# Kernel optimization log

Measured on AMD Instinct MI355X. Metric: run time of the kernel, lower is better.

The kernel has to match this reference:

```python
import jax, jax.numpy as jnp
import numpy as np

BN_EPS = 1e-5


def conv1x1(x, w, b):
    # x: [B,C,H,W], w: [O,C] (squeezed 1x1 kernel), b: [O]
    return jnp.einsum('bchw,oc->bohw', x, w) + b[None, :, None, None]


def setup_inputs() -> dict:
    key = jax.random.key(0)
    ks = jax.random.split(key, 12)
    B, C, H, W = 4, 64, 256, 256
    s = 1.0 / np.sqrt(C).astype(np.float32)
    inp = {
        'x': jax.random.normal(ks[0], (B, C, H, W), jnp.float32),
        'theta_w': jax.random.normal(ks[1], (C, C), jnp.float32) * s,
        'theta_b': jax.random.normal(ks[2], (C,), jnp.float32) * 0.01,
        'phi_w': jax.random.normal(ks[3], (C, C), jnp.float32) * s,
        'phi_b': jax.random.normal(ks[4], (C,), jnp.float32) * 0.01,
        'g_w': jax.random.normal(ks[5], (C, C), jnp.float32) * s,
        'g_b': jax.random.normal(ks[6], (C,), jnp.float32) * 0.01,
        'w_w': jax.random.normal(ks[7], (C, C), jnp.float32) * s,
        'w_b': jax.random.normal(ks[8], (C,), jnp.float32) * 0.01,
        'bn_gamma': jax.random.normal(ks[9], (C,), jnp.float32) * 0.1,
        'bn_beta': jax.random.normal(ks[10], (C,), jnp.float32) * 0.1,
    }
    return inp


def reference(x, theta_w, theta_b, phi_w, phi_b, g_w, g_b, w_w, w_b, bn_gamma, bn_beta):
    B, C, H, W = x.shape
    N = H * W
    g_x = conv1x1(x, g_w, g_b).reshape(B, C, N)          # [B,C,N]
    theta_x = conv1x1(x, theta_w, theta_b).reshape(B, C, N)
    phi_x = conv1x1(x, phi_w, phi_b).reshape(B, C, N)
    # f = phi_x @ theta_x^T : channel-channel affinity [B,C,C]
    f = jnp.einsum('bcn,bdn->bcd', phi_x, theta_x)
    attn = jax.nn.softmax(f, axis=-1)                    # [B,C,C]
    y = jnp.einsum('bcd,bdn->bcn', attn, g_x)            # [B,C,N]
    # faithful to torch: permute(0,2,1).contiguous().view(B,C,H,W)
    y = jnp.transpose(y, (0, 2, 1)).reshape(B, C, H, W)
    w_y = conv1x1(y, w_w, w_b)                           # [B,C,H,W]
    # BatchNorm2d in training mode: batch stats over (B,H,W), biased var
    mean = jnp.mean(w_y, axis=(0, 2, 3), keepdims=True)
    var = jnp.var(w_y, axis=(0, 2, 3), keepdims=True)
    w_y = (w_y - mean) * jax.lax.rsqrt(var + BN_EPS)
    w_y = w_y * bn_gamma[None, :, None, None] + bn_beta[None, :, None, None]
    return w_y + x
```

## Files before the change

kernel.cpp:

```cpp
#include <hip/hip_runtime.h>
#include <hip/hip_bf16.h>
#include <stdint.h>

namespace {

constexpr size_t OFF_G     = 0;
constexpr size_t OFF_S     = 65536;
constexpr size_t OFF_M     = 66560;
constexpr size_t OFF_AB    = 132096;
constexpr size_t OFF_SCALE = 133120;
constexpr size_t OFF_STATS = 133632;
constexpr size_t OFF_WWT   = 134144;
constexpr size_t OFF_WSUM  = 150528;
constexpr size_t OFF_SPART = 150784;
constexpr size_t OFF_GPART = 412928;
constexpr size_t OFF_V     = 17190144;
constexpr size_t OFF_WY    = 50744576;

__device__ __forceinline__ float bf2f(unsigned short u) {
    return __uint_as_float(((unsigned)u) << 16);
}
__device__ __forceinline__ unsigned short f2bf(float f) {
    union { __hip_bfloat16 h; unsigned short u; } cv;
    cv.h = __float2bfloat16(f);
    return cv.u;
}
__device__ __forceinline__ unsigned pack2bf(float a, float b) {
    return (unsigned)f2bf(a) | ((unsigned)f2bf(b) << 16);
}

__global__ __launch_bounds__(256) void k_trans(const float* __restrict__ Ww,
                                               float* __restrict__ WwT,
                                               float* __restrict__ Wsum) {
    const int t = threadIdx.x;
    for (int e = t; e < 4096; e += 256) {
        const int o = e >> 6, c = e & 63;
        WwT[c * 64 + o] = Ww[e];
    }
    if (t < 64) {
        float s = 0.f;
#pragma unroll 8
        for (int c = 0; c < 64; ++c) s += Ww[t * 64 + c];
        Wsum[t] = s;
    }
}

__global__ __launch_bounds__(128) void k_gram(const float* __restrict__ x,
                                              float* __restrict__ gpart,
                                              float* __restrict__ spart) {
    const int wg = blockIdx.x;
    const int b = wg >> 8;
    const int chunk = wg & 255;
    const int t = threadIdx.x;
    const int wv = t >> 6;
    const int l = t & 63;
    const int g = l >> 3, h = l & 7;

    __shared__ __align__(16) float tile[64][64];
    __shared__ __align__(16) float Gred[4096];

    float acc[8][8];
#pragma unroll
    for (int i = 0; i < 8; ++i)
#pragma unroll
        for (int j = 0; j < 8; ++j) acc[i][j] = 0.f;
    float sp[8];
#pragma unroll
    for (int i = 0; i < 8; ++i) sp[i] = 0.f;

    const float* xb = x + (size_t)b * 64 * 65536 + chunk * 256;

    for (int t4 = 0; t4 < 4; ++t4) {
#pragma unroll
        for (int it = 0; it < 8; ++it) {
            const int v = it * 128 + t;
            const int row = v >> 4;
            const int c4 = v & 15;
            const float4 val = *(const float4*)(xb + (size_t)row * 65536 + t4 * 64 + c4 * 4);
            const int c4s = c4 ^ (row >> 3);
            *(float4*)&tile[row][c4s * 4] = val;
            sp[it] += val.x + val.y + val.z + val.w;
        }
        __syncthreads();
        const int fbase = wv * 8;
#pragma unroll
        for (int fs = 0; fs < 8; ++fs) {
            const int f = fbase + fs;
            float4 a4[8], b4[8];
#pragma unroll
            for (int i = 0; i < 8; ++i) a4[i] = *(const float4*)&tile[g * 8 + i][(f ^ g) * 4];
#pragma unroll
            for (int j = 0; j < 8; ++j) b4[j] = *(const float4*)&tile[h * 8 + j][(f ^ h) * 4];
#pragma unroll
            for (int i = 0; i < 8; ++i)
#pragma unroll
                for (int j = 0; j < 8; ++j) {
                    acc[i][j] += a4[i].x * b4[j].x;
                    acc[i][j] += a4[i].y * b4[j].y;
                    acc[i][j] += a4[i].z * b4[j].z;
                    acc[i][j] += a4[i].w * b4[j].w;
                }
        }
        __syncthreads();
    }

    if (wv == 1) {
#pragma unroll
        for (int i = 0; i < 8; ++i)
#pragma unroll
            for (int j4 = 0; j4 < 2; ++j4) {
                float4 v;
                v.x = acc[i][j4 * 4 + 0]; v.y = acc[i][j4 * 4 + 1];
                v.z = acc[i][j4 * 4 + 2]; v.w = acc[i][j4 * 4 + 3];
                *(float4*)&Gred[(g * 8 + i) * 64 + h * 8 + j4 * 4] = v;
            }
    }
    __syncthreads();
    if (wv == 0) {
        float* gp = gpart + (size_t)wg * 4096;
#pragma unroll
        for (int i = 0; i < 8; ++i)
#pragma unroll
            for (int j4 = 0; j4 < 2; ++j4) {
                const float4 r = *(const float4*)&Gred[(g * 8 + i) * 64 + h * 8 + j4 * 4];
                float4 v;
                v.x = acc[i][j4 * 4 + 0] + r.x; v.y = acc[i][j4 * 4 + 1] + r.y;
                v.z = acc[i][j4 * 4 + 2] + r.z; v.w = acc[i][j4 * 4 + 3] + r.w;
                *(float4*)(gp + (g * 8 + i) * 64 + h * 8 + j4 * 4) = v;
            }
    }
#pragma unroll
    for (int it = 0; it < 8; ++it) {
        float v = sp[it];
        v += __shfl_xor(v, 1);
        v += __shfl_xor(v, 2);
        v += __shfl_xor(v, 4);
        v += __shfl_xor(v, 8);
        if ((l & 15) == 0) {
            const int row = it * 8 + (t >> 4);
            spart[((size_t)b * 256 + chunk) * 64 + row] = v;
        }
    }
}

__global__ __launch_bounds__(256) void k_gred(const float* __restrict__ gpart,
                                              const float* __restrict__ spart,
                                              float* __restrict__ G,
                                              float* __restrict__ s) {
    const int b = blockIdx.x >> 4;
    const int part = blockIdx.x & 15;
    const int t = threadIdx.x;
    const int e4l = t & 63;
    const int cg = t >> 6;
    const int e4 = part * 64 + e4l;
    const float4* gp4 = (const float4*)gpart;

    float4 a = make_float4(0.f, 0.f, 0.f, 0.f);
#pragma unroll 8
    for (int i = 0; i < 64; ++i) {
        const int w = cg * 64 + i;
        const float4 v = gp4[((size_t)b * 256 + w) * 1024 + e4];
        a.x += v.x; a.y += v.y; a.z += v.z; a.w += v.w;
    }
    __shared__ __align__(16) float4 red[4][64];
    __shared__ float reds[4][64];
    red[cg][e4l] = a;

    float sv = 0.f;
    if (part == 0) {
#pragma unroll 8
        for (int i = 0; i < 64; ++i) {
            const int w = cg * 64 + i;
            sv += spart[((size_t)b * 256 + w) * 64 + e4l];
        }
        reds[cg][e4l] = sv;
    }
    __syncthreads();
    if (cg == 0) {
        const float4 r1 = red[1][e4l], r2 = red[2][e4l], r3 = red[3][e4l];
        float4 o;
        o.x = a.x + r1.x + r2.x + r3.x;
        o.y = a.y + r1.y + r2.y + r3.y;
        o.z = a.z + r1.z + r2.z + r3.z;
        o.w = a.w + r1.w + r2.w + r3.w;
        *(float4*)(G + (size_t)b * 4096 + (size_t)e4 * 4) = o;
        if (part == 0) {
            s[b * 64 + e4l] = sv + reds[1][e4l] + reds[2][e4l] + reds[3][e4l];
        }
    }
}

__global__ __launch_bounds__(256) void k_small(const float* __restrict__ G,
                                               const float* __restrict__ s,
                                               const float* __restrict__ Pw,
                                               const float* __restrict__ pb,
                                               const float* __restrict__ Tw,
                                               const float* __restrict__ tb,
                                               const float* __restrict__ Gw,
                                               const float* __restrict__ gb,
                                               float* __restrict__ Mt,
                                               float* __restrict__ ab) {
    const int b = blockIdx.x >> 1;
    const int rblk = (blockIdx.x & 1) * 32;
    const int t = threadIdx.x;
    const int rl = t >> 3;
    const int seg = t & 7;
    const int d0 = seg * 8;
    const int rg = rblk + rl;

    __shared__ __align__(16) float GL[64][68];
    __shared__ __align__(16) float TwL[64][68];
    __shared__ __align__(16) float GwL[64][68];
    __shared__ __align__(16) float PwL[32][68];
    __shared__ __align__(16) float AL[32][68];
    __shared__ __align__(16) float atL[32][68];
    __shared__ float sL[64], TsL[64], PsL[32], pbL[64], tbL[64], gbL[64];

    for (int v = t; v < 1024; v += 256) {
        const int k = v >> 4, c4 = (v & 15) * 4;
        *(float4*)&GL[k][c4]  = *(const float4*)(G + (size_t)b * 4096 + (size_t)v * 4);
        *(float4*)&TwL[k][c4] = *(const float4*)(Tw + (size_t)v * 4);
        *(float4*)&GwL[k][c4] = *(const float4*)(Gw + (size_t)v * 4);
    }
    for (int v = t; v < 512; v += 256) {
        const int k = v >> 4, c4 = (v & 15) * 4;
        *(float4*)&PwL[k][c4] = *(const float4*)(Pw + (size_t)(rblk + k) * 64 + c4);
    }
    if (t < 64) {
        sL[t] = s[b * 64 + t];
        pbL[t] = pb[t]; tbL[t] = tb[t]; gbL[t] = gb[t];
    }
    __syncthreads();
    if (t < 64) {
        float a = 0.f;
#pragma unroll 8
        for (int k = 0; k < 64; ++k) a += TwL[t][k] * sL[k];
        TsL[t] = a;
    }
    if (t < 32) {
        float a = 0.f;
#pragma unroll 8
        for (int k = 0; k < 64; ++k) a += PwL[t][k] * sL[k];
        PsL[t] = a;
    }
    {
        float4 a1 = make_float4(0.f, 0.f, 0.f, 0.f), a2 = make_float4(0.f, 0.f, 0.f, 0.f);
#pragma unroll 4
        for (int k = 0; k < 64; ++k) {
            const float pw = PwL[rl][k];
            const float4 g1 = *(const float4*)&GL[k][d0];
            const float4 g2 = *(const float4*)&GL[k][d0 + 4];
            a1.x += pw * g1.x; a1.y += pw * g1.y; a1.z += pw * g1.z; a1.w += pw * g1.w;
            a2.x += pw * g2.x; a2.y += pw * g2.y; a2.z += pw * g2.z; a2.w += pw * g2.w;
        }
        *(float4*)&AL[rl][d0] = a1;
        *(float4*)&AL[rl][d0 + 4] = a2;
    }
    __syncthreads();
    float4 areg[16];
#pragma unroll
    for (int i = 0; i < 16; ++i) areg[i] = *(const float4*)&AL[rl][i * 4];
    float fv[8];
#pragma unroll
    for (int dd = 0; dd < 8; ++dd) {
        const int d = d0 + dd;
        float4 a4 = make_float4(0.f, 0.f, 0.f, 0.f);
#pragma unroll
        for (int i = 0; i < 16; ++i) {
            const float4 tw = *(const float4*)&TwL[d][i * 4];
            a4.x += areg[i].x * tw.x; a4.y += areg[i].y * tw.y;
            a4.z += areg[i].z * tw.z; a4.w += areg[i].w * tw.w;
        }
        const float dot = (a4.x + a4.y) + (a4.z + a4.w);
        fv[dd] = dot + PsL[rl] * tbL[d] + pbL[rg] * (TsL[d] + 65536.f * tbL[d]);
    }
    float mx = fv[0];
#pragma unroll
    for (int dd = 1; dd < 8; ++dd) mx = fmaxf(mx, fv[dd]);
    mx = fmaxf(mx, __shfl_xor(mx, 1));
    mx = fmaxf(mx, __shfl_xor(mx, 2));
    mx = fmaxf(mx, __shfl_xor(mx, 4));
    float sm = 0.f;
#pragma unroll
    for (int dd = 0; dd < 8; ++dd) { fv[dd] = __expf(fv[dd] - mx); sm += fv[dd]; }
    sm += __shfl_xor(sm, 1);
    sm += __shfl_xor(sm, 2);
    sm += __shfl_xor(sm, 4);
    const float inv = 1.f / sm;
    float4 p1, p2;
    p1.x = fv[0] * inv; p1.y = fv[1] * inv; p1.z = fv[2] * inv; p1.w = fv[3] * inv;
    p2.x = fv[4] * inv; p2.y = fv[5] * inv; p2.z = fv[6] * inv; p2.w = fv[7] * inv;
    *(float4*)&atL[rl][d0] = p1;
    *(float4*)&atL[rl][d0 + 4] = p2;
    __syncthreads();
#pragma unroll
    for (int i = 0; i < 16; ++i) areg[i] = *(const float4*)&atL[rl][i * 4];
    float4 m1 = make_float4(0.f, 0.f, 0.f, 0.f), m2 = make_float4(0.f, 0.f, 0.f, 0.f);
    float abv = 0.f;
#pragma unroll
    for (int d4 = 0; d4 < 16; ++d4) {
        const float4 a = areg[d4];
#define MSTEP(comp, dc) { \
        const int d = d4 * 4 + dc; \
        const float ad = a.comp; \
        const float4 g1 = *(const float4*)&GwL[d][d0]; \
        const float4 g2 = *(const float4*)&GwL[d][d0 + 4]; \
        m1.x += ad * g1.x; m1.y += ad * g1.y; m1.z += ad * g1.z; m1.w += ad * g1.w; \
        m2.x += ad * g2.x; m2.y += ad * g2.y; m2.z += ad * g2.z; m2.w += ad * g2.w; \
        abv += ad * gbL[d]; }
        MSTEP(x, 0) MSTEP(y, 1) MSTEP(z, 2) MSTEP(w, 3)
#undef MSTEP
    }
    float mv[8] = {m1.x, m1.y, m1.z, m1.w, m2.x, m2.y, m2.z, m2.w};
    float* Mb = Mt + (size_t)b * 4096;
#pragma unroll
    for (int dd = 0; dd < 8; ++dd) Mb[(d0 + dd) * 64 + rg] = mv[dd];
    if (seg == 0) ab[b * 64 + rg] = abv;
}

__global__ __launch_bounds__(256) void k_convV(const float* __restrict__ x,
                                               const float* __restrict__ WwT,
                                               unsigned short* __restrict__ V) {
    const int bid = blockIdx.x;
    const int b = bid >> 7;
    const int k = (bid >> 1) & 63;
    const int qh = bid & 1;
    const int t = threadIdx.x;
    const int wv = t >> 6;
    const int l = t & 63;
    const int q0 = qh * 512 + l * 8;
    const int o0 = wv * 16;

    __shared__ __align__(16) float WL[64][64];
    {
        const float4* src = (const float4*)WwT;
        float4* dst = (float4*)&WL[0][0];
#pragma unroll
        for (int i = 0; i < 4; ++i) dst[i * 256 + t] = src[i * 256 + t];
    }
    __syncthreads();

    const float* xb = x + ((size_t)b * 64 + k) * 65536 + q0;
    float acc[16][8];
#pragma unroll
    for (int i = 0; i < 16; ++i)
#pragma unroll
        for (int j = 0; j < 8; ++j) acc[i][j] = 0.f;

#pragma unroll 2
    for (int c = 0; c < 64; ++c) {
        const float4 x1 = *(const float4*)(xb + (size_t)c * 1024);
        const float4 x2 = *(const float4*)(xb + (size_t)c * 1024 + 4);
        const float xv[8] = {x1.x, x1.y, x1.z, x1.w, x2.x, x2.y, x2.z, x2.w};
        const float4* wp = (const float4*)&WL[c][o0];
        const float4 w0 = wp[0], w1 = wp[1], w2 = wp[2], w3 = wp[3];
        const float wv16[16] = {w0.x, w0.y, w0.z, w0.w, w1.x, w1.y, w1.z, w1.w,
                                w2.x, w2.y, w2.z, w2.w, w3.x, w3.y, w3.z, w3.w};
#pragma unroll
        for (int i = 0; i < 16; ++i) {
            const float w = wv16[i];
#pragma unroll
            for (int j = 0; j < 8; ++j) acc[i][j] += w * xv[j];
        }
    }
    unsigned short* vb = V + (((size_t)b * 64 + o0) * 64 + k) * 1024 + q0;
#pragma unroll
    for (int i = 0; i < 16; ++i) {
        uint4 pk;
        pk.x = pack2bf(acc[i][0], acc[i][1]);
        pk.y = pack2bf(acc[i][2], acc[i][3]);
        pk.z = pack2bf(acc[i][4], acc[i][5]);
        pk.w = pack2bf(acc[i][6], acc[i][7]);
        *(uint4*)(vb + (size_t)i * 65536) = pk;
    }
}

__global__ __launch_bounds__(256) void k_wy(const unsigned short* __restrict__ V,
                                            const float* __restrict__ Mt,
                                            const float* __restrict__ ab,
                                            const float* __restrict__ Wsum,
                                            const float* __restrict__ wb,
                                            unsigned short* __restrict__ wy,
                                            float* __restrict__ stats) {
    const int bid = blockIdx.x;
    const int b = bid >> 7;
    const int o = (bid >> 1) & 63;
    const int qh = bid & 1;
    const int t = threadIdx.x;
    const int wv = t >> 6;
    const int l = t & 63;
    const int q0 = qh * 512 + l * 8;
    const int r0 = wv * 16;

    __shared__ __align__(16) float MtL[64][64];
    {
        const float4* src = (const float4*)(Mt + (size_t)b * 4096);
        float4* dst = (float4*)&MtL[0][0];
#pragma unroll
        for (int i = 0; i < 4; ++i) dst[i * 256 + t] = src[i * 256 + t];
    }
    __syncthreads();

    const unsigned short* vbase = V + ((size_t)b * 64 + o) * 65536 + q0;
    float acc[16][8];
#pragma unroll
    for (int i = 0; i < 16; ++i)
#pragma unroll
        for (int j = 0; j < 8; ++j) acc[i][j] = 0.f;

#pragma unroll 2
    for (int k = 0; k < 64; ++k) {
        const uint4 u = *(const uint4*)(vbase + (size_t)k * 1024);
        float v[8];
        v[0] = __uint_as_float(u.x << 16);
        v[1] = __uint_as_float(u.x & 0xffff0000u);
        v[2] = __uint_as_float(u.y << 16);
        v[3] = __uint_as_float(u.y & 0xffff0000u);
        v[4] = __uint_as_float(u.z << 16);
        v[5] = __uint_as_float(u.z & 0xffff0000u);
        v[6] = __uint_as_float(u.w << 16);
        v[7] = __uint_as_float(u.w & 0xffff0000u);
        const float4* mp = (const float4*)&MtL[k][r0];
        const float4 m0 = mp[0], m1 = mp[1], m2 = mp[2], m3 = mp[3];
        const float mv16[16] = {m0.x, m0.y, m0.z, m0.w, m1.x, m1.y, m1.z, m1.w,
                                m2.x, m2.y, m2.z, m2.w, m3.x, m3.y, m3.z, m3.w};
#pragma unroll
        for (int i = 0; i < 16; ++i) {
            const float m = mv16[i];
#pragma unroll
            for (int j = 0; j < 8; ++j) acc[i][j] += m * v[j];
        }
    }

    const float wsum_o = Wsum[o];
    const float wb_o = wb[o];
    const float* abb = ab + (size_t)b * 64 + r0;
    float addv[16];
#pragma unroll
    for (int i = 0; i < 16; ++i) addv[i] = wsum_o * abb[i] + wb_o;

    float ssum = 0.f, ssq = 0.f;
#pragma unroll
    for (int i = 0; i < 16; ++i)
#pragma unroll
        for (int j = 0; j < 8; ++j) {
            const float val = acc[i][j] + addv[i];
            acc[i][j] = val;
            ssum += val;
            ssq += val * val;
        }

    unsigned short* wyb = wy + ((size_t)b * 64 + o) * 65536 + (size_t)q0 * 64 + r0;
#pragma unroll
    for (int j = 0; j < 8; ++j) {
        uint4 p1, p2;
        p1.x = pack2bf(acc[0][j],  acc[1][j]);
        p1.y = pack2bf(acc[2][j],  acc[3][j]);
        p1.z = pack2bf(acc[4][j],  acc[5][j]);
        p1.w = pack2bf(acc[6][j],  acc[7][j]);
        p2.x = pack2bf(acc[8][j],  acc[9][j]);
        p2.y = pack2bf(acc[10][j], acc[11][j]);
        p2.z = pack2bf(acc[12][j], acc[13][j]);
        p2.w = pack2bf(acc[14][j], acc[15][j]);
        *(uint4*)(wyb + (size_t)j * 64) = p1;
        *(uint4*)(wyb + (size_t)j * 64 + 8) = p2;
    }

    float v1 = ssum, v2 = ssq;
#pragma unroll
    for (int off = 1; off < 64; off <<= 1) {
        v1 += __shfl_xor(v1, off);
        v2 += __shfl_xor(v2, off);
    }
    if ((t & 63) == 0) {
        atomicAdd(&stats[o], v1);
        atomicAdd(&stats[64 + o], v2);
    }
}

__global__ __launch_bounds__(64) void k_statfin(const float* __restrict__ stats,
                                                const float* __restrict__ gamma,
                                                const float* __restrict__ beta,
                                                float* __restrict__ scaleA,
                                                float* __restrict__ shiftB) {
    const int o = threadIdx.x;
    const float invn = 1.f / 262144.f;
    const float mean = stats[o] * invn;
    const float var = stats[64 + o] * invn - mean * mean;
    const float sA = gamma[o] * rsqrtf(var + 1e-5f);
    scaleA[o] = sA;
    shiftB[o] = beta[o] - mean * sA;
}

__global__ __launch_bounds__(256) void k_out(const unsigned short* __restrict__ wy,
                                             const float* __restrict__ x,
                                             const float* __restrict__ scaleA,
                                             const float* __restrict__ shiftB,
                                             float* __restrict__ out) {
    const size_t stride = (size_t)gridDim.x * blockDim.x;
    for (size_t i8 = (size_t)blockIdx.x * blockDim.x + threadIdx.x; i8 < 2097152; i8 += stride) {
        const size_t base = i8 * 8;
        const int o = (int)((base >> 16) & 63);
        const uint4 u = *(const uint4*)(wy + base);
        const float4 x1 = *(const float4*)(x + base);
        const float4 x2 = *(const float4*)(x + base + 4);
        const float a = scaleA[o];
        const float c = shiftB[o];
        float4 o1, o2;
        o1.x = __uint_as_float(u.x << 16) * a + c + x1.x;
        o1.y = __uint_as_float(u.x & 0xffff0000u) * a + c + x1.y;
        o1.z = __uint_as_float(u.y << 16) * a + c + x1.z;
        o1.w = __uint_as_float(u.y & 0xffff0000u) * a + c + x1.w;
        o2.x = __uint_as_float(u.z << 16) * a + c + x2.x;
        o2.y = __uint_as_float(u.z & 0xffff0000u) * a + c + x2.y;
        o2.z = __uint_as_float(u.w << 16) * a + c + x2.z;
        o2.w = __uint_as_float(u.w & 0xffff0000u) * a + c + x2.w;
        *(float4*)(out + base) = o1;
        *(float4*)(out + base + 4) = o2;
    }
}

}

extern "C" void kernel_launch(void* const* d_in, const int* in_sizes, int n_in,
                              void* d_out, int out_size, void* d_ws, size_t ws_size,
                              hipStream_t stream) {
    const float* x        = (const float*)d_in[0];
    const float* theta_w  = (const float*)d_in[1];
    const float* theta_b  = (const float*)d_in[2];
    const float* phi_w    = (const float*)d_in[3];
    const float* phi_b    = (const float*)d_in[4];
    const float* g_w      = (const float*)d_in[5];
    const float* g_b      = (const float*)d_in[6];
    const float* w_w      = (const float*)d_in[7];
    const float* w_b      = (const float*)d_in[8];
    const float* bn_gamma = (const float*)d_in[9];
    const float* bn_beta  = (const float*)d_in[10];
    float* out = (float*)d_out;
    char* ws = (char*)d_ws;

    float* G      = (float*)(ws + OFF_G);
    float* s      = (float*)(ws + OFF_S);
    float* Mt     = (float*)(ws + OFF_M);
    float* ab     = (float*)(ws + OFF_AB);
    float* scaleA = (float*)(ws + OFF_SCALE);
    float* shiftB = scaleA + 64;
    float* stats  = (float*)(ws + OFF_STATS);
    float* WwT    = (float*)(ws + OFF_WWT);
    float* Wsum   = (float*)(ws + OFF_WSUM);
    float* spart  = (float*)(ws + OFF_SPART);
    float* gpart  = (float*)(ws + OFF_GPART);
    unsigned short* V  = (unsigned short*)(ws + OFF_V);
    unsigned short* wy = (unsigned short*)(ws + OFF_WY);

    (void)in_sizes; (void)n_in; (void)out_size; (void)ws_size;

    hipMemsetAsync(stats, 0, 512, stream);
    hipLaunchKernelGGL(k_trans, dim3(1), dim3(256), 0, stream, w_w, WwT, Wsum);
    hipLaunchKernelGGL(k_gram, dim3(1024), dim3(128), 0, stream, x, gpart, spart);
    hipLaunchKernelGGL(k_gred, dim3(64), dim3(256), 0, stream, gpart, spart, G, s);
    hipLaunchKernelGGL(k_small, dim3(8), dim3(256), 0, stream, G, s, phi_w, phi_b,
                       theta_w, theta_b, g_w, g_b, Mt, ab);
    hipLaunchKernelGGL(k_convV, dim3(512), dim3(256), 0, stream, x, WwT, V);
    hipLaunchKernelGGL(k_wy, dim3(512), dim3(256), 0, stream, V, Mt, ab, Wsum, w_b, wy, stats);
    hipLaunchKernelGGL(k_statfin, dim3(1), dim3(64), 0, stream, stats, bn_gamma, bn_beta,
                       scaleA, shiftB);
    hipLaunchKernelGGL(k_out, dim3(2048), dim3(256), 0, stream, wy, x, scaleA, shiftB, out);
}
```

Baseline: 282.7 us.

## Compute Gram matrix with split-bf16 MFMA instead of fp32 FMA

Rewrites the per-chunk Gram kernel to load x directly from global memory into registers, split each float into bf16 hi and lo parts, and accumulate x·xᵀ with 16x16x32 bf16 MFMA instructions (hi*hi + hi*lo + lo*hi) across four waves, each owning a 32x32 quadrant. It drops the LDS tile staging and the cross-wave LDS reduction and doubles the block size. The aim is to replace the scalar FP32 FMA work with matrix-core throughput. In exchange, precision drops slightly because the lo*lo term is omitted, each row is loaded redundantly by several waves, and the global reads are strided.

```diff
diff --git a/kernel.cpp b/kernel.cpp
--- a/kernel.cpp
+++ b/kernel.cpp
@@ -17,6 +17,9 @@
 constexpr size_t OFF_V     = 17190144;
 constexpr size_t OFF_WY    = 50744576;
 
+typedef __attribute__((ext_vector_type(8))) short bf16x8;
+typedef __attribute__((ext_vector_type(4))) float f32x4;
+
 __device__ __forceinline__ float bf2f(unsigned short u) {
     return __uint_as_float(((unsigned)u) << 16);
 }
@@ -27,6 +30,22 @@
 }
 __device__ __forceinline__ unsigned pack2bf(float a, float b) {
     return (unsigned)f2bf(a) | ((unsigned)f2bf(b) << 16);
+}
+
+__device__ __forceinline__ void loadcvt(const float* __restrict__ p,
+                                        bf16x8& hi, bf16x8& lo, float& sum) {
+    const float4 v1 = *(const float4*)p;
+    const float4 v2 = *(const float4*)(p + 4);
+    const float f[8] = {v1.x, v1.y, v1.z, v1.w, v2.x, v2.y, v2.z, v2.w};
+    float s = 0.f;
+#pragma unroll
+    for (int j = 0; j < 8; ++j) {
+        s += f[j];
+        const unsigned short h = f2bf(f[j]);
+        hi[j] = (short)h;
+        lo[j] = (short)f2bf(f[j] - bf2f(h));
+    }
+    sum = s;
 }
 
 __global__ __launch_bounds__(256) void k_trans(const float* __restrict__ Ww,
@@ -45,101 +64,76 @@
     }
 }
 
-__global__ __launch_bounds__(128) void k_gram(const float* __restrict__ x,
+__global__ __launch_bounds__(256) void k_gram(const float* __restrict__ x,
                                               float* __restrict__ gpart,
                                               float* __restrict__ spart) {
     const int wg = blockIdx.x;
     const int b = wg >> 8;
     const int chunk = wg & 255;
     const int t = threadIdx.x;
-    const int wv = t >> 6;
+    const int w = t >> 6;
     const int l = t & 63;
-    const int g = l >> 3, h = l & 7;
-
-    __shared__ __align__(16) float tile[64][64];
-    __shared__ __align__(16) float Gred[4096];
-
-    float acc[8][8];
-#pragma unroll
-    for (int i = 0; i < 8; ++i)
-#pragma unroll
-        for (int j = 0; j < 8; ++j) acc[i][j] = 0.f;
-    float sp[8];
-#pragma unroll
-    for (int i = 0; i < 8; ++i) sp[i] = 0.f;
-
-    const float* xb = x + (size_t)b * 64 * 65536 + chunk * 256;
-
-    for (int t4 = 0; t4 < 4; ++t4) {
-#pragma unroll
-        for (int it = 0; it < 8; ++it) {
-            const int v = it * 128 + t;
-            const int row = v >> 4;
-            const int c4 = v & 15;
-            const float4 val = *(const float4*)(xb + (size_t)row * 65536 + t4 * 64 + c4 * 4);
-            const int c4s = c4 ^ (row >> 3);
-            *(float4*)&tile[row][c4s * 4] = val;
-            sp[it] += val.x + val.y + val.z + val.w;
-        }
-        __syncthreads();
-        const int fbase = wv * 8;
-#pragma unroll
-        for (int fs = 0; fs < 8; ++fs) {
-            const int f = fbase + fs;
-            float4 a4[8], b4[8];
-#pragma unroll
-            for (int i = 0; i < 8; ++i) a4[i] = *(const float4*)&tile[g * 8 + i][(f ^ g) * 4];
-#pragma unroll
-            for (int j = 0; j < 8; ++j) b4[j] = *(const float4*)&tile[h * 8 + j][(f ^ h) * 4];
-#pragma unroll
-            for (int i = 0; i < 8; ++i)
-#pragma unroll
-                for (int j = 0; j < 8; ++j) {
-                    acc[i][j] += a4[i].x * b4[j].x;
-                    acc[i][j] += a4[i].y * b4[j].y;
-                    acc[i][j] += a4[i].z * b4[j].z;
-                    acc[i][j] += a4[i].w * b4[j].w;
-                }
-        }
-        __syncthreads();
-    }
-
-    if (wv == 1) {
-#pragma unroll
-        for (int i = 0; i < 8; ++i)
-#pragma unroll
-            for (int j4 = 0; j4 < 2; ++j4) {
-                float4 v;
-                v.x = acc[i][j4 * 4 + 0]; v.y = acc[i][j4 * 4 + 1];
-                v.z = acc[i][j4 * 4 + 2]; v.w = acc[i][j4 * 4 + 3];
-                *(float4*)&Gred[(g * 8 + i) * 64 + h * 8 + j4 * 4] = v;
-            }
-    }
-    __syncthreads();
-    if (wv == 0) {
-        float* gp = gpart + (size_t)wg * 4096;
-#pragma unroll
-        for (int i = 0; i < 8; ++i)
-#pragma unroll
-            for (int j4 = 0; j4 < 2; ++j4) {
-                const float4 r = *(const float4*)&Gred[(g * 8 + i) * 64 + h * 8 + j4 * 4];
-                float4 v;
-                v.x = acc[i][j4 * 4 + 0] + r.x; v.y = acc[i][j4 * 4 + 1] + r.y;
-                v.z = acc[i][j4 * 4 + 2] + r.z; v.w = acc[i][j4 * 4 + 3] + r.w;
-                *(float4*)(gp + (g * 8 + i) * 64 + h * 8 + j4 * 4) = v;
-            }
-    }
-#pragma unroll
-    for (int it = 0; it < 8; ++it) {
-        float v = sp[it];
-        v += __shfl_xor(v, 1);
-        v += __shfl_xor(v, 2);
-        v += __shfl_xor(v, 4);
-        v += __shfl_xor(v, 8);
-        if ((l & 15) == 0) {
-            const int row = it * 8 + (t >> 4);
-            spart[((size_t)b * 256 + chunk) * 64 + row] = v;
-        }
+    const int wr = w >> 1, wc = w & 1;
+    const int lr = l & 15;
+    const int lk = l >> 4;
+
+    const float* xb = x + (size_t)b * 64 * 65536 + chunk * 256 + lk * 8;
+    const float* pa0 = xb + (size_t)(wr * 32 + lr) * 65536;
+    const float* pa1 = xb + (size_t)(wr * 32 + 16 + lr) * 65536;
+    const float* pb0 = xb + (size_t)(wc * 32 + lr) * 65536;
+    const float* pb1 = xb + (size_t)(wc * 32 + 16 + lr) * 65536;
+
+    f32x4 acc00 = {0.f, 0.f, 0.f, 0.f};
+    f32x4 acc01 = {0.f, 0.f, 0.f, 0.f};
+    f32x4 acc10 = {0.f, 0.f, 0.f, 0.f};
+    f32x4 acc11 = {0.f, 0.f, 0.f, 0.f};
+    float sA0 = 0.f, sA1 = 0.f;
+
+#pragma unroll 2
+    for (int ks = 0; ks < 8; ++ks) {
+        const int off = ks * 32;
+        bf16x8 ah0, al0, ah1, al1, bh0, bl0, bh1, bl1;
+        float s0, s1, sd;
+        loadcvt(pa0 + off, ah0, al0, s0); sA0 += s0;
+        loadcvt(pa1 + off, ah1, al1, s1); sA1 += s1;
+        loadcvt(pb0 + off, bh0, bl0, sd);
+        loadcvt(pb1 + off, bh1, bl1, sd);
+
+        acc00 = __builtin_amdgcn_mfma_f32_16x16x32_bf16(ah0, bh0, acc00, 0, 0, 0);
+        acc00 = __builtin_amdgcn_mfma_f32_16x16x32_bf16(ah0, bl0, acc00, 0, 0, 0);
+        acc00 = __builtin_amdgcn_mfma_f32_16x16x32_bf16(al0, bh0, acc00, 0, 0, 0);
+
+        acc01 = __builtin_amdgcn_mfma_f32_16x16x32_bf16(ah0, bh1, acc01, 0, 0, 0);
+        acc01 = __builtin_amdgcn_mfma_f32_16x16x32_bf16(ah0, bl1, acc01, 0, 0, 0);
+        acc01 = __builtin_amdgcn_mfma_f32_16x16x32_bf16(al0, bh1, acc01, 0, 0, 0);
+
+        acc10 = __builtin_amdgcn_mfma_f32_16x16x32_bf16(ah1, bh0, acc10, 0, 0, 0);
+        acc10 = __builtin_amdgcn_mfma_f32_16x16x32_bf16(ah1, bl0, acc10, 0, 0, 0);
+        acc10 = __builtin_amdgcn_mfma_f32_16x16x32_bf16(al1, bh0, acc10, 0, 0, 0);
+
+        acc11 = __builtin_amdgcn_mfma_f32_16x16x32_bf16(ah1, bh1, acc11, 0, 0, 0);
+        acc11 = __builtin_amdgcn_mfma_f32_16x16x32_bf16(ah1, bl1, acc11, 0, 0, 0);
+        acc11 = __builtin_amdgcn_mfma_f32_16x16x32_bf16(al1, bh1, acc11, 0, 0, 0);
+    }
+
+    float* gp = gpart + (size_t)wg * 4096;
+    {
+        const int c0 = wc * 32 + lr;
+        const int r00 = wr * 32 + lk * 4;
+#pragma unroll
+        for (int r = 0; r < 4; ++r) {
+            gp[(r00 + r) * 64 + c0]           = acc00[r];
+            gp[(r00 + r) * 64 + c0 + 16]      = acc01[r];
+            gp[(r00 + 16 + r) * 64 + c0]      = acc10[r];
+            gp[(r00 + 16 + r) * 64 + c0 + 16] = acc11[r];
+        }
+    }
+    sA0 += __shfl_xor(sA0, 16); sA0 += __shfl_xor(sA0, 32);
+    sA1 += __shfl_xor(sA1, 16); sA1 += __shfl_xor(sA1, 32);
+    if (wc == 0 && l < 16) {
+        float* sp = spart + (size_t)wg * 64 + wr * 32;
+        sp[l] = sA0;
+        sp[16 + l] = sA1;
     }
 }
 
@@ -557,7 +551,7 @@
 
     hipMemsetAsync(stats, 0, 512, stream);
     hipLaunchKernelGGL(k_trans, dim3(1), dim3(256), 0, stream, w_w, WwT, Wsum);
-    hipLaunchKernelGGL(k_gram, dim3(1024), dim3(128), 0, stream, x, gpart, spart);
+    hipLaunchKernelGGL(k_gram, dim3(1024), dim3(256), 0, stream, x, gpart, spart);
     hipLaunchKernelGGL(k_gred, dim3(64), dim3(256), 0, stream, gpart, spart, G, s);
     hipLaunchKernelGGL(k_small, dim3(8), dim3(256), 0, stream, G, s, phi_w, phi_b,
                        theta_w, theta_b, g_w, g_b, Mt, ab);
```

New measurement: 278.4 us. About the same (-1.5%).
